# Optimization experiments

Measured on AMD Instinct MI355X. Metric: run time of the kernel, lower is better.

The kernel has to match this reference:

```python
import jax, jax.numpy as jnp
import numpy as np

EPS = 1e-5

def _ln(x, gamma, beta):
    mu = jnp.mean(x, axis=-1, keepdims=True)
    var = jnp.mean(jnp.square(x - mu), axis=-1, keepdims=True)
    return (x - mu) * jax.lax.rsqrt(var + EPS) * gamma + beta

def _linear(x, w, b):
    # torch nn.Linear convention: w is [out, in]
    return jnp.einsum('...i,oi->...o', x, w) + b

def setup_inputs() -> dict:
    key = jax.random.key(0)
    B, L, C = 1, 384, 128
    ks = jax.random.split(key, 16)
    s = 1.0 / np.sqrt(C)
    inp = {
        'pair_feat': jax.random.normal(ks[0], (B, L, L, C), dtype=jnp.float32),
        'res_mask': jnp.ones((B, L), dtype=jnp.float32),
        # left_proj: Linear + LayerNorm
        'lp_w': jax.random.uniform(ks[1], (C, C), jnp.float32, -s, s),
        'lp_b': jnp.zeros((C,), jnp.float32),
        'lp_g': jnp.ones((C,), jnp.float32),
        'lp_beta': jnp.zeros((C,), jnp.float32),
        # right_proj: Linear + LayerNorm
        'rp_w': jax.random.uniform(ks[2], (C, C), jnp.float32, -s, s),
        'rp_b': jnp.zeros((C,), jnp.float32),
        'rp_g': jnp.ones((C,), jnp.float32),
        'rp_beta': jnp.zeros((C,), jnp.float32),
        # gates: Linear (then sigmoid)
        'lg_w': jax.random.uniform(ks[3], (C, C), jnp.float32, -s, s),
        'lg_b': jnp.zeros((C,), jnp.float32),
        'rg_w': jax.random.uniform(ks[4], (C, C), jnp.float32, -s, s),
        'rg_b': jnp.zeros((C,), jnp.float32),
        'og_w': jax.random.uniform(ks[5], (C, C), jnp.float32, -s, s),
        'og_b': jnp.zeros((C,), jnp.float32),
        # out_layer: LayerNorm + Linear
        'ol_g': jnp.ones((C,), jnp.float32),
        'ol_beta': jnp.zeros((C,), jnp.float32),
        'ow': jax.random.uniform(ks[6], (C, C), jnp.float32, -s, s),
        'ob': jnp.zeros((C,), jnp.float32),
    }
    return inp

def reference(pair_feat, res_mask, lp_w, lp_b, lp_g, lp_beta,
              rp_w, rp_b, rp_g, rp_beta, lg_w, lg_b, rg_w, rg_b,
              og_w, og_b, ol_g, ol_beta, ow, ob):
    # op_type == 'outgoing': einsum 'bikc,bjkc->bijc'
    proj_left = _ln(_linear(pair_feat, lp_w, lp_b), lp_g, lp_beta)
    proj_right = _ln(_linear(pair_feat, rp_w, rp_b), rp_g, rp_beta)
    mask2d = (res_mask[:, :, None] * res_mask[:, None, :])[..., None]  # [B,L,L,1]
    proj_left = proj_left * mask2d
    proj_right = proj_right * mask2d
    gate_left = jax.nn.sigmoid(_linear(pair_feat, lg_w, lg_b))
    gate_right = jax.nn.sigmoid(_linear(pair_feat, rg_w, rg_b))
    proj_left = proj_left * gate_left
    proj_right = proj_right * gate_right
    out = jnp.einsum('bikc,bjkc->bijc', proj_left, proj_right)
    out = _linear(_ln(out, ol_g, ol_beta), ow, ob)
    gate = jax.nn.sigmoid(_linear(pair_feat, og_w, og_b))
    return out * gate
```

## Files before the change

kernel.cpp:

```cpp
#include <hip/hip_runtime.h>

typedef __bf16 bf16x8 __attribute__((ext_vector_type(8)));
typedef __bf16 bf16x4 __attribute__((ext_vector_type(4)));
typedef float  f32x4  __attribute__((ext_vector_type(4)));
typedef int    int4v  __attribute__((ext_vector_type(4)));

#define LL    384
#define CC    128
#define NROW  (LL * LL)

#define MFMA16(a, b, c) __builtin_amdgcn_mfma_f32_16x16x32_bf16((a), (b), (c), 0, 0, 0)

__device__ __forceinline__ bf16x8 cvt8(const float* p) {
    f32x4 a = *reinterpret_cast<const f32x4*>(p);
    f32x4 b = *reinterpret_cast<const f32x4*>(p + 4);
    bf16x8 r;
    r[0] = (__bf16)a[0]; r[1] = (__bf16)a[1]; r[2] = (__bf16)a[2]; r[3] = (__bf16)a[3];
    r[4] = (__bf16)b[0]; r[5] = (__bf16)b[1]; r[6] = (__bf16)b[2]; r[7] = (__bf16)b[3];
    return r;
}
__device__ __forceinline__ bf16x8 ld_ws(const __bf16* p) {
    return __builtin_bit_cast(bf16x8, *reinterpret_cast<const int4v*>(p));
}
__device__ __forceinline__ float sigmf(float x) { return 1.f / (1.f + __expf(-x)); }

__device__ __forceinline__ void gl16(const __bf16* g, __bf16* l) {
    __builtin_amdgcn_global_load_lds(
        (const __attribute__((address_space(1))) unsigned int*)g,
        (__attribute__((address_space(3))) unsigned int*)l,
        16, 0, 0);
}

__device__ __forceinline__ void stage_weight(const float* __restrict__ w,
                                             __bf16* dst, int tid) {
    const int c   = tid >> 1;
    const int k0  = (tid & 1) * 64;
    const int nt  = c >> 4;
    const int n16 = c & 15;
    #pragma unroll
    for (int u = 0; u < 8; ++u) {
        const int k    = k0 + u * 8;
        const int ks   = k >> 5;
        const int quad = (k >> 3) & 3;
        bf16x8 v = cvt8(w + c * CC + k);
        *reinterpret_cast<int4v*>(dst + ((ks * 8 + nt) * 64 + quad * 16 + n16) * 8) =
            __builtin_bit_cast(int4v, v);
    }
}
__device__ __forceinline__ bf16x8 wfrag(const __bf16* base, int ks, int nt, int lane) {
    return ld_ws(base + ((ks * 8 + nt) * 64 + lane) * 8);
}

__global__ __launch_bounds__(256) void k_wconv(
    const float* __restrict__ w0, const float* __restrict__ w1,
    const float* __restrict__ w2, const float* __restrict__ w3,
    const float* __restrict__ w4, const float* __restrict__ w5,
    __bf16* __restrict__ dst)
{
    const float* srcs[6] = {w0, w1, w2, w3, w4, w5};
    stage_weight(srcs[blockIdx.x], dst + (size_t)blockIdx.x * 16384, threadIdx.x);
}

__global__ __launch_bounds__(256, 3) void k_proj(
    const float* __restrict__ pf, const float* __restrict__ rmask,
    const __bf16* __restrict__ wfm,
    const float* __restrict__ lp_b, const float* __restrict__ lp_g,
    const float* __restrict__ lp_be,
    const float* __restrict__ rp_b, const float* __restrict__ rp_g,
    const float* __restrict__ rp_be,
    const float* __restrict__ lg_b, const float* __restrict__ rg_b,
    __bf16* __restrict__ pl_c, __bf16* __restrict__ pr_c)
{
    __shared__ __bf16 wl[16384];

    const int tid  = threadIdx.x;
    const int wave = tid >> 6, lane = tid & 63;
    const int n16  = lane & 15, quad = lane >> 4;
    const int rowbase = blockIdx.x * 64 + wave * 16;

    auto STAGEW = [&](int widx) {
        const __bf16* src = wfm + (size_t)widx * 16384;
        #pragma unroll
        for (int i = 0; i < 8; ++i) {
            const int s = wave * 8 + i;
            gl16(src + (size_t)s * 512 + lane * 8, wl + (size_t)s * 512);
        }
    };

    bf16x8 xf[4];
    #pragma unroll
    for (int ks = 0; ks < 4; ++ks)
        xf[ks] = cvt8(pf + (size_t)(rowbase + n16) * CC + ks * 32 + quad * 8);

    float mrow[4];
    {
        const int rd   = rowbase + quad * 4;
        const int i_id = rd / LL;
        const int k_id = rd - i_id * LL;
        float mi = rmask[i_id];
        #pragma unroll
        for (int g = 0; g < 4; ++g) mrow[g] = mi * rmask[k_id + g];
    }

    f32x4 acc[8];
    auto GEMM = [&]() {
        #pragma unroll
        for (int nt = 0; nt < 8; ++nt) acc[nt] = f32x4{0.f, 0.f, 0.f, 0.f};
        #pragma unroll
        for (int ks = 0; ks < 4; ++ks)
            #pragma unroll
            for (int nt = 0; nt < 8; ++nt) {
                bf16x8 wf = wfrag(wl, ks, nt, lane);
                acc[nt] = MFMA16(xf[ks], wf, acc[nt]);
            }
    };

    bf16x4 sg[8];
    auto SIGM = [&](const float* gb) {
        #pragma unroll
        for (int nt = 0; nt < 8; ++nt) {
            float bias = gb[nt * 16 + n16];
            #pragma unroll
            for (int g = 0; g < 4; ++g)
                sg[nt][g] = (__bf16)sigmf(acc[nt][g] + bias);
        }
    };

    auto EPILOG = [&](const float* pb, const float* gamma, const float* beta,
                      __bf16* dst) {
        #pragma unroll
        for (int nt = 0; nt < 8; ++nt) {
            float bias = pb[nt * 16 + n16];
            #pragma unroll
            for (int g = 0; g < 4; ++g) acc[nt][g] += bias;
        }
        float s[4] = {0.f,0.f,0.f,0.f}, ss[4] = {0.f,0.f,0.f,0.f};
        #pragma unroll
        for (int nt = 0; nt < 8; ++nt)
            #pragma unroll
            for (int g = 0; g < 4; ++g) { float v = acc[nt][g]; s[g] += v; ss[g] += v * v; }
        #pragma unroll
        for (int m = 1; m < 16; m <<= 1)
            #pragma unroll
            for (int g = 0; g < 4; ++g) {
                s[g]  += __shfl_xor(s[g],  m, 64);
                ss[g] += __shfl_xor(ss[g], m, 64);
            }
        float mean[4], rstd[4];
        #pragma unroll
        for (int g = 0; g < 4; ++g) {
            mean[g] = s[g] * (1.f / 128.f);
            float var = ss[g] * (1.f / 128.f) - mean[g] * mean[g];
            rstd[g] = rsqrtf(fmaxf(var, 0.f) + 1e-5f);
        }
        const int rd = rowbase + quad * 4;
        #pragma unroll
        for (int nt = 0; nt < 8; ++nt) {
            const int c = nt * 16 + n16;
            float ga = gamma[c], be = beta[c];
            bf16x4 o;
            #pragma unroll
            for (int g = 0; g < 4; ++g) {
                float v = (acc[nt][g] - mean[g]) * rstd[g] * ga + be;
                v *= mrow[g] * (float)sg[nt][g];
                o[g] = (__bf16)v;
            }
            *reinterpret_cast<bf16x4*>(dst + (size_t)c * NROW + rd) = o;
        }
    };

    STAGEW(0);
    __syncthreads();

    GEMM();
    __syncthreads();
    STAGEW(1);
    SIGM(lg_b);
    __syncthreads();

    GEMM();
    __syncthreads();
    STAGEW(2);
    EPILOG(lp_b, lp_g, lp_be, pl_c);
    __syncthreads();

    GEMM();
    __syncthreads();
    STAGEW(3);
    SIGM(rg_b);
    __syncthreads();

    GEMM();
    EPILOG(rp_b, rp_g, rp_be, pr_c);
}

__global__ __launch_bounds__(256, 3) void k_einsum_tile(
    const __bf16* __restrict__ pl_c, const __bf16* __restrict__ pr_c,
    float* __restrict__ T)
{
    __shared__ __bf16 sA[2][512 * 8];
    __shared__ __bf16 sB[2][512 * 8];

    const int bid  = blockIdx.x;
    const int wgid = (bid & 7) * 144 + (bid >> 3);
    const int ch   = wgid / 9;
    const int tile = wgid - ch * 9;
    const int i0   = (tile / 3) * 128;
    const int j0   = (tile % 3) * 128;

    const int tid  = threadIdx.x;
    const int w    = tid >> 6, lane = tid & 63;
    const int n16  = lane & 15, quad = lane >> 4;
    const int wr   = w >> 1, wc = w & 1;

    const __bf16* Pc = pl_c + (size_t)ch * NROW;
    const __bf16* Qc = pr_c + (size_t)ch * NROW;

    const __bf16* ga[2];
    const __bf16* gb[2];
    #pragma unroll
    for (int u = 0; u < 2; ++u) {
        const int row = (w * 2 + u) * 16 + n16;
        ga[u] = Pc + (size_t)(i0 + row) * LL + quad * 8;
        gb[u] = Qc + (size_t)(j0 + row) * LL + quad * 8;
    }

    f32x4 acc[4][4];
    #pragma unroll
    for (int m = 0; m < 4; ++m)
        #pragma unroll
        for (int n = 0; n < 4; ++n) acc[m][n] = f32x4{0.f, 0.f, 0.f, 0.f};

    auto STAGE = [&](int buf, int k0) {
        #pragma unroll
        for (int u = 0; u < 2; ++u) {
            __bf16* la = &sA[buf][(size_t)((w * 2 + u) * 64) * 8];
            __bf16* lb = &sB[buf][(size_t)((w * 2 + u) * 64) * 8];
            gl16(ga[u] + k0, la);
            gl16(gb[u] + k0, lb);
        }
    };

    STAGE(0, 0);
    __syncthreads();

    #pragma unroll
    for (int t = 0; t < 12; ++t) {
        if (t < 11) STAGE((t + 1) & 1, (t + 1) * 32);
        const __bf16* Ab = sA[t & 1];
        const __bf16* Bb = sB[t & 1];
        bf16x8 af[4], bf[4];
        #pragma unroll
        for (int m = 0; m < 4; ++m) af[m] = ld_ws(Ab + ((size_t)((wr * 4 + m) * 64 + lane)) * 8);
        #pragma unroll
        for (int n = 0; n < 4; ++n) bf[n] = ld_ws(Bb + ((size_t)((wc * 4 + n) * 64 + lane)) * 8);
        #pragma unroll
        for (int m = 0; m < 4; ++m)
            #pragma unroll
            for (int n = 0; n < 4; ++n)
                acc[m][n] = MFMA16(af[m], bf[n], acc[m][n]);
        __syncthreads();
    }

    float* Tc = T + (size_t)ch * NROW;
    #pragma unroll
    for (int m = 0; m < 4; ++m) {
        const int i = i0 + wr * 64 + m * 16 + quad * 4;
        #pragma unroll
        for (int n = 0; n < 4; ++n) {
            const int j = j0 + wc * 64 + n * 16 + n16;
            #pragma unroll
            for (int g = 0; g < 4; ++g)
                Tc[(size_t)(i + g) * LL + j] = acc[m][n][g];
        }
    }
}

__global__ __launch_bounds__(256, 2) void k_final_cm(
    float* __restrict__ out, const float* __restrict__ T,
    const float* __restrict__ pf, const __bf16* __restrict__ wfm,
    const float* __restrict__ ol_g, const float* __restrict__ ol_be,
    const float* __restrict__ ob,   const float* __restrict__ og_b)
{
    __shared__ __bf16 wl[2][16384];
    const int tid  = threadIdx.x;
    const int wave = tid >> 6, lane = tid & 63;
    const int n16  = lane & 15, quad = lane >> 4;
    const int rowblock = blockIdx.x * 128 + wave * 32;

    #pragma unroll
    for (int i = 0; i < 8; ++i) {
        const int s = wave * 8 + i;
        gl16(wfm + (size_t)(4 * 16384) + (size_t)s * 512 + lane * 8, wl[0] + (size_t)s * 512);
        gl16(wfm + (size_t)(5 * 16384) + (size_t)s * 512 + lane * 8, wl[1] + (size_t)s * 512);
    }
    __syncthreads();

    #pragma unroll
    for (int rg = 0; rg < 2; ++rg) {
        const int r = rowblock + rg * 16 + n16;

        f32x4 tf[8];
        bf16x8 pff[4];
        #pragma unroll
        for (int ks = 0; ks < 4; ++ks) {
            #pragma unroll
            for (int q = 0; q < 4; ++q) {
                tf[2 * ks][q]     = T[(size_t)(ks * 32 + quad * 8 + q)     * NROW + r];
                tf[2 * ks + 1][q] = T[(size_t)(ks * 32 + quad * 8 + 4 + q) * NROW + r];
            }
            pff[ks] = cvt8(pf + (size_t)r * CC + ks * 32 + quad * 8);
        }

        float s = 0.f, ss = 0.f;
        #pragma unroll
        for (int h = 0; h < 8; ++h)
            #pragma unroll
            for (int q = 0; q < 4; ++q) { float f = tf[h][q]; s += f; ss += f * f; }
        s += __shfl_xor(s, 16, 64);  ss += __shfl_xor(ss, 16, 64);
        s += __shfl_xor(s, 32, 64);  ss += __shfl_xor(ss, 32, 64);
        const float mean = s * (1.f / 128.f);
        const float rstd = rsqrtf(fmaxf(ss * (1.f / 128.f) - mean * mean, 0.f) + 1e-5f);

        bf16x8 xn[4];
        #pragma unroll
        for (int ks = 0; ks < 4; ++ks) {
            const int cb = ks * 32 + quad * 8;
            f32x4 g0 = *reinterpret_cast<const f32x4*>(ol_g + cb);
            f32x4 g1 = *reinterpret_cast<const f32x4*>(ol_g + cb + 4);
            f32x4 b0 = *reinterpret_cast<const f32x4*>(ol_be + cb);
            f32x4 b1 = *reinterpret_cast<const f32x4*>(ol_be + cb + 4);
            bf16x8 rv;
            #pragma unroll
            for (int q = 0; q < 4; ++q) {
                rv[q]     = (__bf16)((tf[2 * ks][q]     - mean) * rstd * g0[q] + b0[q]);
                rv[4 + q] = (__bf16)((tf[2 * ks + 1][q] - mean) * rstd * g1[q] + b1[q]);
            }
            xn[ks] = rv;
        }

        f32x4 ao[8], ag[8];
        #pragma unroll
        for (int mt = 0; mt < 8; ++mt) { ao[mt] = f32x4{0.f,0.f,0.f,0.f}; ag[mt] = f32x4{0.f,0.f,0.f,0.f}; }
        #pragma unroll
        for (int ks = 0; ks < 4; ++ks)
            #pragma unroll
            for (int mt = 0; mt < 8; ++mt) {
                bf16x8 awf = wfrag(wl[0], ks, mt, lane);
                bf16x8 gwf = wfrag(wl[1], ks, mt, lane);
                ao[mt] = MFMA16(awf, xn[ks],  ao[mt]);
                ag[mt] = MFMA16(gwf, pff[ks], ag[mt]);
            }

        #pragma unroll
        for (int mt = 0; mt < 8; ++mt) {
            const int c0 = mt * 16 + quad * 4;
            f32x4 bb = *reinterpret_cast<const f32x4*>(ob + c0);
            f32x4 gb = *reinterpret_cast<const f32x4*>(og_b + c0);
            f32x4 o;
            #pragma unroll
            for (int g = 0; g < 4; ++g) {
                float gate = sigmf(ag[mt][g] + gb[g]);
                o[g] = (ao[mt][g] + bb[g]) * gate;
            }
            *reinterpret_cast<f32x4*>(out + (size_t)r * CC + c0) = o;
        }
    }
}

__global__ __launch_bounds__(256, 2) void k_proj_fb(
    const float* __restrict__ pf, const float* __restrict__ rmask,
    const float* __restrict__ lp_w, const float* __restrict__ lp_b,
    const float* __restrict__ lp_g, const float* __restrict__ lp_be,
    const float* __restrict__ rp_w, const float* __restrict__ rp_b,
    const float* __restrict__ rp_g, const float* __restrict__ rp_be,
    const float* __restrict__ lg_w, const float* __restrict__ lg_b,
    const float* __restrict__ rg_w, const float* __restrict__ rg_b,
    __bf16* __restrict__ pl_c, __bf16* __restrict__ pr_c)
{
    __shared__ __bf16 wl[2 * 16384];

    const int tid  = threadIdx.x;
    const int wave = tid >> 6, lane = tid & 63;
    const int n16  = lane & 15, quad = lane >> 4;
    const int rowblock = blockIdx.x * 128 + wave * 32;

    bf16x8 xf[2][4];
    #pragma unroll
    for (int rg = 0; rg < 2; ++rg) {
        const int r_a = rowblock + rg * 16 + n16;
        #pragma unroll
        for (int ks = 0; ks < 4; ++ks)
            xf[rg][ks] = cvt8(pf + (size_t)r_a * CC + ks * 32 + quad * 8);
    }

    float mrow[2][4];
    #pragma unroll
    for (int rg = 0; rg < 2; ++rg) {
        const int rd   = rowblock + rg * 16 + quad * 4;
        const int i_id = rd / LL;
        const int k_id = rd - i_id * LL;
        float mi = rmask[i_id];
        #pragma unroll
        for (int g = 0; g < 4; ++g) mrow[rg][g] = mi * rmask[k_id + g];
    }

    auto phase = [&](const float* gw, const float* gb,
                     const float* pw, const float* pb,
                     const float* gamma, const float* beta,
                     __bf16* dst) {
        stage_weight(gw, wl, tid);
        stage_weight(pw, wl + 16384, tid);
        __syncthreads();

        f32x4 acc[2][8];
        #pragma unroll
        for (int rg = 0; rg < 2; ++rg)
            #pragma unroll
            for (int nt = 0; nt < 8; ++nt) acc[rg][nt] = f32x4{0.f, 0.f, 0.f, 0.f};
        #pragma unroll
        for (int ks = 0; ks < 4; ++ks)
            #pragma unroll
            for (int nt = 0; nt < 8; ++nt) {
                bf16x8 wf = wfrag(wl, ks, nt, lane);
                #pragma unroll
                for (int rg = 0; rg < 2; ++rg)
                    acc[rg][nt] = MFMA16(xf[rg][ks], wf, acc[rg][nt]);
            }
        bf16x4 sg[2][8];
        #pragma unroll
        for (int rg = 0; rg < 2; ++rg)
            #pragma unroll
            for (int nt = 0; nt < 8; ++nt) {
                float bias = gb[nt * 16 + n16];
                #pragma unroll
                for (int g = 0; g < 4; ++g)
                    sg[rg][nt][g] = (__bf16)sigmf(acc[rg][nt][g] + bias);
            }
        #pragma unroll
        for (int rg = 0; rg < 2; ++rg)
            #pragma unroll
            for (int nt = 0; nt < 8; ++nt) acc[rg][nt] = f32x4{0.f, 0.f, 0.f, 0.f};
        #pragma unroll
        for (int ks = 0; ks < 4; ++ks)
            #pragma unroll
            for (int nt = 0; nt < 8; ++nt) {
                bf16x8 wf = wfrag(wl + 16384, ks, nt, lane);
                #pragma unroll
                for (int rg = 0; rg < 2; ++rg)
                    acc[rg][nt] = MFMA16(xf[rg][ks], wf, acc[rg][nt]);
            }
        #pragma unroll
        for (int rg = 0; rg < 2; ++rg) {
            #pragma unroll
            for (int nt = 0; nt < 8; ++nt) {
                float bias = pb[nt * 16 + n16];
                #pragma unroll
                for (int g = 0; g < 4; ++g) acc[rg][nt][g] += bias;
            }
            float s[4] = {0.f,0.f,0.f,0.f}, ss[4] = {0.f,0.f,0.f,0.f};
            #pragma unroll
            for (int nt = 0; nt < 8; ++nt)
                #pragma unroll
                for (int g = 0; g < 4; ++g) { float v = acc[rg][nt][g]; s[g] += v; ss[g] += v * v; }
            #pragma unroll
            for (int m = 1; m < 16; m <<= 1)
                #pragma unroll
                for (int g = 0; g < 4; ++g) {
                    s[g]  += __shfl_xor(s[g],  m, 64);
                    ss[g] += __shfl_xor(ss[g], m, 64);
                }
            float mean[4], rstd[4];
            #pragma unroll
            for (int g = 0; g < 4; ++g) {
                mean[g] = s[g] * (1.f / 128.f);
                float var = ss[g] * (1.f / 128.f) - mean[g] * mean[g];
                rstd[g] = rsqrtf(fmaxf(var, 0.f) + 1e-5f);
            }
            const int rd = rowblock + rg * 16 + quad * 4;
            #pragma unroll
            for (int nt = 0; nt < 8; ++nt) {
                const int c = nt * 16 + n16;
                float ga = gamma[c], be = beta[c];
                bf16x4 o;
                #pragma unroll
                for (int g = 0; g < 4; ++g) {
                    float v = (acc[rg][nt][g] - mean[g]) * rstd[g] * ga + be;
                    v *= mrow[rg][g] * (float)sg[rg][nt][g];
                    o[g] = (__bf16)v;
                }
                *reinterpret_cast<bf16x4*>(dst + (size_t)c * NROW + rd) = o;
            }
        }
        __syncthreads();
    };

    phase(lg_w, lg_b, lp_w, lp_b, lp_g, lp_be, pl_c);
    phase(rg_w, rg_b, rp_w, rp_b, rp_g, rp_be, pr_c);
}

__global__ __launch_bounds__(256, 2) void k_einsum_direct(
    const __bf16* __restrict__ pl_c, const __bf16* __restrict__ pr_c,
    float* __restrict__ out)
{
    const int tid  = threadIdx.x;
    const int wave = tid >> 6, lane = tid & 63;
    const int n16  = lane & 15, quad = lane >> 4;
    const int i0   = blockIdx.x * 64;
    const int jw   = blockIdx.y * 64 + wave * 16;
    const int c0   = blockIdx.z * 8;

    size_t off_i[4];
    #pragma unroll
    for (int t = 0; t < 4; ++t)
        off_i[t] = (size_t)(i0 + t * 16 + n16) * LL + quad * 8;
    const size_t off_j = (size_t)(jw + n16) * LL + quad * 8;

    f32x4 acc[8][4];
    #pragma unroll
    for (int c = 0; c < 8; ++c)
        #pragma unroll
        for (int t = 0; t < 4; ++t) acc[c][t] = f32x4{0.f, 0.f, 0.f, 0.f};

    #pragma unroll
    for (int c = 0; c < 8; ++c) {
        const __bf16* Pb = pl_c + (size_t)(c0 + c) * NROW;
        const __bf16* Qb = pr_c + (size_t)(c0 + c) * NROW + off_j;
        #pragma unroll
        for (int kt = 0; kt < 12; ++kt) {
            bf16x8 fj = ld_ws(Qb + kt * 32);
            #pragma unroll
            for (int t = 0; t < 4; ++t) {
                bf16x8 fi = ld_ws(Pb + off_i[t] + kt * 32);
                acc[c][t] = MFMA16(fi, fj, acc[c][t]);
            }
        }
    }

    #pragma unroll
    for (int t = 0; t < 4; ++t)
        #pragma unroll
        for (int g = 0; g < 4; ++g) {
            const int i = i0 + t * 16 + quad * 4 + g;
            float* dst = out + ((size_t)i * LL + jw + n16) * CC + c0;
            f32x4 lo, hi;
            #pragma unroll
            for (int q = 0; q < 4; ++q) { lo[q] = acc[q][t][g]; hi[q] = acc[4 + q][t][g]; }
            *reinterpret_cast<f32x4*>(dst)     = lo;
            *reinterpret_cast<f32x4*>(dst + 4) = hi;
        }
}

__global__ __launch_bounds__(256, 2) void k_final_ip(
    float* out, const float* __restrict__ pf,
    const float* __restrict__ ol_g, const float* __restrict__ ol_be,
    const float* __restrict__ ow,   const float* __restrict__ ob,
    const float* __restrict__ og_w, const float* __restrict__ og_b)
{
    __shared__ __bf16 wl[2 * 16384];
    const int tid  = threadIdx.x;
    const int wave = tid >> 6, lane = tid & 63;
    const int n16  = lane & 15, quad = lane >> 4;
    const int rowblock = blockIdx.x * 128 + wave * 32;

    stage_weight(ow,   wl,         tid);
    stage_weight(og_w, wl + 16384, tid);
    __syncthreads();

    #pragma unroll
    for (int rg = 0; rg < 2; ++rg) {
        const int r = rowblock + rg * 16 + n16;

        f32x4 tf[8];
        bf16x8 pff[4];
        #pragma unroll
        for (int ks = 0; ks < 4; ++ks) {
            const float* tp = out + (size_t)r * CC + ks * 32 + quad * 8;
            tf[2 * ks]     = *reinterpret_cast<const f32x4*>(tp);
            tf[2 * ks + 1] = *reinterpret_cast<const f32x4*>(tp + 4);
            pff[ks] = cvt8(pf + (size_t)r * CC + ks * 32 + quad * 8);
        }

        float s = 0.f, ss = 0.f;
        #pragma unroll
        for (int h = 0; h < 8; ++h)
            #pragma unroll
            for (int q = 0; q < 4; ++q) { float f = tf[h][q]; s += f; ss += f * f; }
        s += __shfl_xor(s, 16, 64);  ss += __shfl_xor(ss, 16, 64);
        s += __shfl_xor(s, 32, 64);  ss += __shfl_xor(ss, 32, 64);
        const float mean = s * (1.f / 128.f);
        const float rstd = rsqrtf(fmaxf(ss * (1.f / 128.f) - mean * mean, 0.f) + 1e-5f);

        bf16x8 xn[4];
        #pragma unroll
        for (int ks = 0; ks < 4; ++ks) {
            const int cb = ks * 32 + quad * 8;
            f32x4 g0 = *reinterpret_cast<const f32x4*>(ol_g + cb);
            f32x4 g1 = *reinterpret_cast<const f32x4*>(ol_g + cb + 4);
            f32x4 b0 = *reinterpret_cast<const f32x4*>(ol_be + cb);
            f32x4 b1 = *reinterpret_cast<const f32x4*>(ol_be + cb + 4);
            bf16x8 rv;
            #pragma unroll
            for (int q = 0; q < 4; ++q) {
                rv[q]     = (__bf16)((tf[2 * ks][q]     - mean) * rstd * g0[q] + b0[q]);
                rv[4 + q] = (__bf16)((tf[2 * ks + 1][q] - mean) * rstd * g1[q] + b1[q]);
            }
            xn[ks] = rv;
        }

        f32x4 ao[8], ag[8];
        #pragma unroll
        for (int mt = 0; mt < 8; ++mt) { ao[mt] = f32x4{0.f,0.f,0.f,0.f}; ag[mt] = f32x4{0.f,0.f,0.f,0.f}; }
        #pragma unroll
        for (int ks = 0; ks < 4; ++ks)
            #pragma unroll
            for (int mt = 0; mt < 8; ++mt) {
                bf16x8 awf = wfrag(wl,         ks, mt, lane);
                bf16x8 gwf = wfrag(wl + 16384, ks, mt, lane);
                ao[mt] = MFMA16(awf, xn[ks],  ao[mt]);
                ag[mt] = MFMA16(gwf, pff[ks], ag[mt]);
            }

        #pragma unroll
        for (int mt = 0; mt < 8; ++mt) {
            const int c0 = mt * 16 + quad * 4;
            f32x4 bb = *reinterpret_cast<const f32x4*>(ob + c0);
            f32x4 gb = *reinterpret_cast<const f32x4*>(og_b + c0);
            f32x4 o;
            #pragma unroll
            for (int g = 0; g < 4; ++g) {
                float gate = sigmf(ag[mt][g] + gb[g]);
                o[g] = (ao[mt][g] + bb[g]) * gate;
            }
            *reinterpret_cast<f32x4*>(out + (size_t)r * CC + c0) = o;
        }
    }
}

extern "C" void kernel_launch(void* const* d_in, const int* in_sizes, int n_in,
                              void* d_out, int out_size, void* d_ws, size_t ws_size,
                              hipStream_t stream)
{
    const float* pf    = (const float*)d_in[0];
    const float* rmask = (const float*)d_in[1];
    const float* lp_w  = (const float*)d_in[2];
    const float* lp_b  = (const float*)d_in[3];
    const float* lp_g  = (const float*)d_in[4];
    const float* lp_be = (const float*)d_in[5];
    const float* rp_w  = (const float*)d_in[6];
    const float* rp_b  = (const float*)d_in[7];
    const float* rp_g  = (const float*)d_in[8];
    const float* rp_be = (const float*)d_in[9];
    const float* lg_w  = (const float*)d_in[10];
    const float* lg_b  = (const float*)d_in[11];
    const float* rg_w  = (const float*)d_in[12];
    const float* rg_b  = (const float*)d_in[13];
    const float* og_w  = (const float*)d_in[14];
    const float* og_b  = (const float*)d_in[15];
    const float* ol_g  = (const float*)d_in[16];
    const float* ol_be = (const float*)d_in[17];
    const float* ow    = (const float*)d_in[18];
    const float* ob    = (const float*)d_in[19];
    float* out = (float*)d_out;

    __bf16* pl_c = (__bf16*)d_ws;
    __bf16* pr_c = pl_c + (size_t)CC * NROW;
    __bf16* wfm  = pr_c + (size_t)CC * NROW;
    float*  T    = (float*)(wfm + 6 * 16384);

    const size_t need = (size_t)CC * NROW * (2 + 2 + 4) + 6 * 16384 * 2;

    if (ws_size >= need) {
        k_wconv<<<6, 256, 0, stream>>>(lg_w, lp_w, rg_w, rp_w, ow, og_w, wfm);
        k_proj<<<NROW / 64, 256, 0, stream>>>(pf, rmask, wfm,
            lp_b, lp_g, lp_be, rp_b, rp_g, rp_be, lg_b, rg_b, pl_c, pr_c);
        k_einsum_tile<<<1152, 256, 0, stream>>>(pl_c, pr_c, T);
        k_final_cm<<<NROW / 128, 256, 0, stream>>>(out, T, pf, wfm,
            ol_g, ol_be, ob, og_b);
    } else {
        k_proj_fb<<<NROW / 128, 256, 0, stream>>>(pf, rmask,
            lp_w, lp_b, lp_g, lp_be, rp_w, rp_b, rp_g, rp_be,
            lg_w, lg_b, rg_w, rg_b, pl_c, pr_c);
        k_einsum_direct<<<dim3(LL / 64, LL / 64, CC / 8), 256, 0, stream>>>(pl_c, pr_c, out);
        k_final_ip<<<NROW / 128, 256, 0, stream>>>(out, pf,
            ol_g, ol_be, ow, ob, og_w, og_b);
    }
}
```

Before: 314.4 us.

## Make projection kernel persistent with all four weights resident in LDS

Rewrites k_proj as a persistent kernel with 256 blocks of 512 threads. Each block loads all four projection/gate weight matrices into LDS once and then loops over 36 row tiles per wave-group. The next tile's fp32 inputs are prefetched into registers while the current tile is computed. This removes the repeated weight staging and the barriers between the four GEMMs, at the cost of 128KB of LDS per block and lower occupancy.

After: 680.8 us. 2.17x slower.

```diff
diff --git a/kernel.cpp b/kernel.cpp
--- a/kernel.cpp
+++ b/kernel.cpp
@@ -61,7 +61,7 @@
     stage_weight(srcs[blockIdx.x], dst + (size_t)blockIdx.x * 16384, threadIdx.x);
 }
 
-__global__ __launch_bounds__(256, 3) void k_proj(
+__global__ __launch_bounds__(512, 2) void k_proj(
     const float* __restrict__ pf, const float* __restrict__ rmask,
     const __bf16* __restrict__ wfm,
     const float* __restrict__ lp_b, const float* __restrict__ lp_g,
@@ -71,46 +71,41 @@
     const float* __restrict__ lg_b, const float* __restrict__ rg_b,
     __bf16* __restrict__ pl_c, __bf16* __restrict__ pr_c)
 {
-    __shared__ __bf16 wl[16384];
+    __shared__ __bf16 wl[4 * 16384];
 
     const int tid  = threadIdx.x;
     const int wave = tid >> 6, lane = tid & 63;
     const int n16  = lane & 15, quad = lane >> 4;
-    const int rowbase = blockIdx.x * 64 + wave * 16;
-
-    auto STAGEW = [&](int widx) {
-        const __bf16* src = wfm + (size_t)widx * 16384;
-        #pragma unroll
-        for (int i = 0; i < 8; ++i) {
-            const int s = wave * 8 + i;
-            gl16(src + (size_t)s * 512 + lane * 8, wl + (size_t)s * 512);
+
+    #pragma unroll
+    for (int i = 0; i < 16; ++i) {
+        const int s = wave * 16 + i;
+        gl16(wfm + (size_t)s * 512 + lane * 8, wl + (size_t)s * 512);
+    }
+    __syncthreads();
+
+    const int tile0 = blockIdx.x * 36;
+
+    f32x4 xr[8];
+    auto LOADX = [&](int t) {
+        const float* p = pf + (size_t)(t * 16 + n16) * CC + quad * 8;
+        #pragma unroll
+        for (int ks = 0; ks < 4; ++ks) {
+            xr[2 * ks]     = *reinterpret_cast<const f32x4*>(p + ks * 32);
+            xr[2 * ks + 1] = *reinterpret_cast<const f32x4*>(p + ks * 32 + 4);
         }
     };
 
+    f32x4 acc[8];
     bf16x8 xf[4];
-    #pragma unroll
-    for (int ks = 0; ks < 4; ++ks)
-        xf[ks] = cvt8(pf + (size_t)(rowbase + n16) * CC + ks * 32 + quad * 8);
-
-    float mrow[4];
-    {
-        const int rd   = rowbase + quad * 4;
-        const int i_id = rd / LL;
-        const int k_id = rd - i_id * LL;
-        float mi = rmask[i_id];
-        #pragma unroll
-        for (int g = 0; g < 4; ++g) mrow[g] = mi * rmask[k_id + g];
-    }
-
-    f32x4 acc[8];
-    auto GEMM = [&]() {
+    auto GEMM = [&](const __bf16* wb) {
         #pragma unroll
         for (int nt = 0; nt < 8; ++nt) acc[nt] = f32x4{0.f, 0.f, 0.f, 0.f};
         #pragma unroll
         for (int ks = 0; ks < 4; ++ks)
             #pragma unroll
             for (int nt = 0; nt < 8; ++nt) {
-                bf16x8 wf = wfrag(wl, ks, nt, lane);
+                bf16x8 wf = wfrag(wb, ks, nt, lane);
                 acc[nt] = MFMA16(xf[ks], wf, acc[nt]);
             }
     };
@@ -126,7 +121,8 @@
         }
     };
 
-    auto EPILOG = [&](const float* pb, const float* gamma, const float* beta,
+    auto EPILOG = [&](int rd, const float* mrow,
+                      const float* pb, const float* gamma, const float* beta,
                       __bf16* dst) {
         #pragma unroll
         for (int nt = 0; nt < 8; ++nt) {
@@ -153,7 +149,6 @@
             float var = ss[g] * (1.f / 128.f) - mean[g] * mean[g];
             rstd[g] = rsqrtf(fmaxf(var, 0.f) + 1e-5f);
         }
-        const int rd = rowbase + quad * 4;
         #pragma unroll
         for (int nt = 0; nt < 8; ++nt) {
             const int c = nt * 16 + n16;
@@ -169,29 +164,36 @@
         }
     };
 
-    STAGEW(0);
-    __syncthreads();
-
-    GEMM();
-    __syncthreads();
-    STAGEW(1);
-    SIGM(lg_b);
-    __syncthreads();
-
-    GEMM();
-    __syncthreads();
-    STAGEW(2);
-    EPILOG(lp_b, lp_g, lp_be, pl_c);
-    __syncthreads();
-
-    GEMM();
-    __syncthreads();
-    STAGEW(3);
-    SIGM(rg_b);
-    __syncthreads();
-
-    GEMM();
-    EPILOG(rp_b, rp_g, rp_be, pr_c);
+    int i = wave;
+    if (i < 36) LOADX(tile0 + i);
+    for (; i < 36; i += 8) {
+        const int t = tile0 + i;
+
+        #pragma unroll
+        for (int ks = 0; ks < 4; ++ks) {
+            bf16x8 r;
+            #pragma unroll
+            for (int q = 0; q < 4; ++q) {
+                r[q]     = (__bf16)xr[2 * ks][q];
+                r[4 + q] = (__bf16)xr[2 * ks + 1][q];
+            }
+            xf[ks] = r;
+        }
+        if (i + 8 < 36) LOADX(tile0 + i + 8);
+
+        const int rd   = t * 16 + quad * 4;
+        const int i_id = rd / LL;
+        const int k_id = rd - i_id * LL;
+        float mi = rmask[i_id];
+        float mrow[4];
+        #pragma unroll
+        for (int g = 0; g < 4; ++g) mrow[g] = mi * rmask[k_id + g];
+
+        GEMM(wl);              SIGM(lg_b);
+        GEMM(wl + 16384);      EPILOG(rd, mrow, lp_b, lp_g, lp_be, pl_c);
+        GEMM(wl + 2 * 16384);  SIGM(rg_b);
+        GEMM(wl + 3 * 16384);  EPILOG(rd, mrow, rp_b, rp_g, rp_be, pr_c);
+    }
 }
 
 __global__ __launch_bounds__(256, 3) void k_einsum_tile(
@@ -672,7 +674,7 @@
 
     if (ws_size >= need) {
         k_wconv<<<6, 256, 0, stream>>>(lg_w, lp_w, rg_w, rp_w, ow, og_w, wfm);
-        k_proj<<<NROW / 64, 256, 0, stream>>>(pf, rmask, wfm,
+        k_proj<<<256, 512, 0, stream>>>(pf, rmask, wfm,
             lp_b, lp_g, lp_be, rp_b, rp_g, rp_be, lg_b, rg_b, pl_c, pr_c);
         k_einsum_tile<<<1152, 256, 0, stream>>>(pl_c, pr_c, T);
         k_final_cm<<<NROW / 128, 256, 0, stream>>>(out, T, pf, wfm,
```
